# Optimization experiments

Hardware: AMD Instinct MI355X
Metric: run time of the kernel (lower is better)

## Reference

```python
import jax, jax.numpy as jnp
import numpy as np

EPS = 1e-08
STRIDE = 1


def setup_inputs() -> dict:
    key = jax.random.key(0)
    k_x, k_s, k_sw, k_w = jax.random.split(key, 4)
    B, Cin, Cout, D = 8, 32, 32, 48
    style_size, K = 2, 3
    x = jax.random.normal(k_x, (B, Cin, D, D, D), dtype=jnp.float32)
    s = jax.random.normal(k_s, (B, style_size), dtype=jnp.float32)
    # lecun_normal-style scaling for params
    style_weight = jax.random.normal(k_sw, (Cin, style_size), dtype=jnp.float32) / np.sqrt(style_size)
    style_bias = jnp.ones((Cin,), dtype=jnp.float32)
    weight = jax.random.normal(k_w, (Cout, Cin, K, K, K), dtype=jnp.float32) / np.sqrt(Cin * K * K * K)
    bias = jnp.zeros((Cout,), dtype=jnp.float32)
    return {"x": x, "s": s, "style_weight": style_weight,
            "style_bias": style_bias, "weight": weight, "bias": bias}


def reference(x, s, style_weight, style_bias, weight, bias):
    # Style modulation: per-sample per-input-channel scale  (B, Cin)
    s_mod = jnp.dot(s, style_weight.T) + style_bias
    # Modulated weights: (B, Cout, Cin, K, K, K)
    w = weight[None] * s_mod[:, None, :, None, None, None]
    # Demodulation over (Cin, K, K, K) per (B, Cout)
    norm = jnp.sqrt(jnp.sum(w ** 2, axis=(2, 3, 4, 5), keepdims=True) + jnp.float32(EPS))
    w_n = w / norm

    def single_conv(x_i, w_i):
        # x_i: (Cin, D, H, W), w_i: (Cout, Cin, K, K, K)
        out = jax.lax.conv_general_dilated(
            lhs=x_i[None], rhs=w_i,
            window_strides=(STRIDE,) * 3, padding='VALID',
            dimension_numbers=('NCDHW', 'OIDHW', 'NCDHW'))
        return out[0]

    y = jax.vmap(single_conv)(x, w_n)  # (B, Cout, D', H', W')
    return y + bias[None, :, None, None, None]
```

## Files before the change

### kernel.cpp

```cpp
#include <hip/hip_runtime.h>


typedef unsigned short u16;
typedef __bf16 bf16x8 __attribute__((ext_vector_type(8)));
typedef u16 u16x8 __attribute__((ext_vector_type(8)));
typedef float f32x4 __attribute__((ext_vector_type(4)));

#define XT_BYTES  (8u * 110592u * 32u * 2u)
#define WA2_ELEMS (8 * 32 * 27 * 32)

__device__ __forceinline__ u16 f2bf(float f) {
    __bf16 h = (__bf16)f;
    return __builtin_bit_cast(u16, h);
}

__device__ __forceinline__ void dma16(const void* g, void* l) {
    __builtin_amdgcn_global_load_lds(
        (const __attribute__((address_space(1))) unsigned*)g,
        (__attribute__((address_space(3))) unsigned*)l, 16, 0, 0);
}

__global__ __launch_bounds__(256) void xpose_kernel(
    const float* __restrict__ x, u16* __restrict__ xT)
{
    int gid = blockIdx.x * 256 + threadIdx.x;
    int cg   = gid & 3;
    int tmp  = gid >> 2;
    int quad = tmp % 27648;
    int b    = tmp / 27648;
    int site0 = quad * 4;
    const float* xp = x + (size_t)(b * 32 + cg * 8) * 110592 + site0;
    float4 v[8];
#pragma unroll
    for (int j = 0; j < 8; ++j) v[j] = *(const float4*)(xp + (size_t)j * 110592);
#pragma unroll
    for (int k = 0; k < 4; ++k) {
        u16x8 o;
#pragma unroll
        for (int j = 0; j < 8; ++j) o[j] = f2bf(((const float*)&v[j])[k]);
        *(u16x8*)(xT + ((size_t)(b * 110592 + site0 + k) * 4 + cg) * 8) = o;
    }
}

__global__ __launch_bounds__(64) void wnorm32_kernel(
    const float* __restrict__ s, const float* __restrict__ sw,
    const float* __restrict__ sb, const float* __restrict__ w,
    u16* __restrict__ wA2)
{
    int bc = blockIdx.x;
    int b = bc >> 5, co = bc & 31;
    int lane = threadIdx.x;
    float s0 = s[2 * b], s1 = s[2 * b + 1];

    float sum = 0.f;
    for (int i = lane; i < 864; i += 64) {
        int ci = i / 27;
        float m = fmaf(s0, sw[2 * ci], fmaf(s1, sw[2 * ci + 1], sb[ci]));
        float v = w[co * 864 + i] * m;
        sum += v * v;
    }
#pragma unroll
    for (int off = 32; off; off >>= 1) sum += __shfl_xor(sum, off, 64);
    float rn = 1.0f / sqrtf(sum + 1e-8f);

    for (int i = lane; i < 864; i += 64) {
        int ci = i / 27, tap = i - ci * 27;
        float m = fmaf(s0, sw[2 * ci], fmaf(s1, sw[2 * ci + 1], sb[ci]));
        float v = w[co * 864 + i] * m * rn;
        wA2[((size_t)(b * 32 + co) * 27 + tap) * 32 + ci] = f2bf(v);
    }
}

__global__ __launch_bounds__(512) void conv_one(
    const u16* __restrict__ xT, const u16* __restrict__ wA2,
    const float* __restrict__ bias, float* __restrict__ out)
{
    __shared__ u16 sx[57600];

    int orig = blockIdx.x;
    int blk = (orig & 7) * 144 + (orig >> 3);

    int zt = blk % 12, yt = (blk / 12) % 12, b = blk / 144;
    int z0 = zt * 4, y0 = yt * 4;

    int t = threadIdx.x;
    int l = t & 63, w = t >> 6;
    int ln = l & 15;
    int tq = l >> 4;
    int zw = w & 3, yp = (w >> 2) & 1;

#pragma unroll
    for (int i = 0; i < 15; ++i) {
        int idx = i * 512 + t;
        if (idx < 7200) {
            int site = idx >> 2, slot = idx & 3;
            int row = site / 50, x = site - row * 50;
            int zp = row / 6, yq = row - zp * 6;
            int gz = z0 + zp; if (gz > 47) gz = 47;
            int gy = y0 + yq; if (gy > 47) gy = 47;
            int gx = x > 47 ? 47 : x;
            int rot = (row + (x >> 1)) & 3;
            int g = slot ^ rot;
            const u16* src = xT + ((size_t)(b * 110592 + (gz * 48 + gy) * 48 + gx) * 4 + g) * 8;
            dma16(src, (char*)sx + (size_t)idx * 16);
        }
    }
    __syncthreads();

    f32x4 acc[2][3][2];
#pragma unroll
    for (int i = 0; i < 2; i++)
#pragma unroll
        for (int j = 0; j < 3; j++)
#pragma unroll
            for (int h = 0; h < 2; h++) acc[i][j][h] = (f32x4)0.f;

    const u16* wAb = wA2 + (size_t)(b * 32) * 27 * 32;

#pragma unroll
    for (int dz = 0; dz < 3; ++dz) {
#pragma unroll
        for (int dx = 0; dx < 3; ++dx) {
            u16x8 Bf[4][3];
#pragma unroll
            for (int r = 0; r < 4; ++r) {
                int rowi = (zw + dz) * 6 + 2 * yp + r;
#pragma unroll
                for (int xt = 0; xt < 3; ++xt) {
                    int xx = xt * 16 + ln + dx;
                    int site = rowi * 50 + xx;
                    int rot = (rowi + ((ln + dx) >> 1)) & 3;
                    int boff = site * 64 + ((tq ^ rot) << 4);
                    Bf[r][xt] = *(const u16x8*)((const char*)sx + boff);
                }
            }
            u16x8 Af[3][2];
#pragma unroll
            for (int dy = 0; dy < 3; ++dy) {
                int tap = (dz * 3 + dy) * 3 + dx;
#pragma unroll
                for (int h = 0; h < 2; ++h)
                    Af[dy][h] = *(const u16x8*)(wAb
                        + ((size_t)(ln + 16 * h) * 27 + tap) * 32 + tq * 8);
            }
#pragma unroll
            for (int dy = 0; dy < 3; ++dy)
#pragma unroll
                for (int yr = 0; yr < 2; ++yr)
#pragma unroll
                    for (int xt = 0; xt < 3; ++xt)
#pragma unroll
                        for (int h = 0; h < 2; ++h)
                            acc[yr][xt][h] = __builtin_amdgcn_mfma_f32_16x16x32_bf16(
                                __builtin_bit_cast(bf16x8, Af[dy][h]),
                                __builtin_bit_cast(bf16x8, Bf[yr + dy][xt]),
                                acc[yr][xt][h], 0, 0, 0);
        }
    }

    int oz = z0 + zw;
    if (oz < 46) {
#pragma unroll
        for (int yr = 0; yr < 2; ++yr) {
            int oy = y0 + 2 * yp + yr;
            if (oy >= 46) continue;
#pragma unroll
            for (int xt = 0; xt < 3; ++xt) {
                int ox = xt * 16 + ln;
                if (ox >= 46) continue;
#pragma unroll
                for (int h = 0; h < 2; ++h) {
                    f32x4 a = acc[yr][xt][h];
#pragma unroll
                    for (int r = 0; r < 4; ++r) {
                        int co = h * 16 + tq * 4 + r;
                        out[(size_t)(b * 32 + co) * 97336 + oz * 2116 + oy * 46 + ox]
                            = a[r] + bias[co];
                    }
                }
            }
        }
    }
}

__global__ __launch_bounds__(64) void wnorm16_kernel(
    const float* __restrict__ s, const float* __restrict__ sw,
    const float* __restrict__ sb, const float* __restrict__ w,
    u16* __restrict__ wA)
{
    int bc = blockIdx.x;
    int b = bc >> 5, co = bc & 31;
    int lane = threadIdx.x;
    float s0 = s[2 * b], s1 = s[2 * b + 1];

    float sum = 0.f;
    for (int i = lane; i < 864; i += 64) {
        int ci = i / 27;
        float m = fmaf(s0, sw[2 * ci], fmaf(s1, sw[2 * ci + 1], sb[ci]));
        float v = w[co * 864 + i] * m;
        sum += v * v;
    }
#pragma unroll
    for (int off = 32; off; off >>= 1) sum += __shfl_xor(sum, off, 64);
    float rn = 1.0f / sqrtf(sum + 1e-8f);

    for (int i = lane; i < 864; i += 64) {
        int ci = i / 27, tap = i - ci * 27;
        float m = fmaf(s0, sw[2 * ci], fmaf(s1, sw[2 * ci + 1], sb[ci]));
        float v = w[co * 864 + i] * m * rn;
        int chunk = ci >> 4, ci16 = ci & 15;
        wA[(((b * 2 + chunk) * 32 + co) * 28 + tap) * 16 + ci16] = f2bf(v);
    }
    if (lane < 32) {
        int c = lane >> 4, ci16 = lane & 15;
        wA[(((b * 2 + c) * 32 + co) * 28 + 27) * 16 + ci16] = 0;
    }
}

__global__ __launch_bounds__(512) void conv_fallback(
    const float* __restrict__ xin, const u16* __restrict__ wA,
    const float* __restrict__ bias, float* __restrict__ out)
{
    __shared__ u16 sx[28800];

    int blk = blockIdx.x;
    int zt = blk % 12, yt = (blk / 12) % 12, b = blk / 144;
    int z0 = zt * 4, y0 = yt * 4;

    int t = threadIdx.x;
    int l = t & 63, w = t >> 6;
    int ln = l & 15, ch = (l >> 4) & 1, tp = l >> 5, rg = l >> 4;
    int zw = w & 3, yp = w >> 2;

    f32x4 acc[2][3][2];
#pragma unroll
    for (int i = 0; i < 2; i++)
#pragma unroll
        for (int j = 0; j < 3; j++)
#pragma unroll
            for (int h = 0; h < 2; h++) acc[i][j][h] = (f32x4)0.f;

    for (int chunk = 0; chunk < 2; ++chunk) {
        __syncthreads();
        for (int idx = t; idx < 3600; idx += 512) {
            int x = idx % 50;
            int r = idx / 50;
            int cg = r & 1; r >>= 1;
            int y = r % 6, z = r / 6;
            int gz = z0 + z, gy = y0 + y;
            bool inb = (x < 48) && (gy < 48) && (gz < 48);
            const float* xp = xin + (size_t)(b * 32 + chunk * 16 + cg * 8) * 110592
                              + gz * 2304 + gy * 48 + x;
            u16x8 v;
#pragma unroll
            for (int j = 0; j < 8; j++) {
                float f = inb ? xp[(size_t)j * 110592] : 0.f;
                v[j] = f2bf(f);
            }
            *(u16x8*)&sx[idx * 8] = v;
        }
        __syncthreads();

        const u16* wAc = wA + (b * 2 + chunk) * (32 * 28 * 16);
        int aoff = (ln * 28 + tp) * 16 + ch * 8;

#pragma unroll
        for (int s = 0; s < 14; ++s) {
            int tapA = 2 * s + tp;
            bf16x8 A0 = __builtin_bit_cast(bf16x8, *(const u16x8*)(wAc + aoff + s * 32));
            bf16x8 A1 = __builtin_bit_cast(bf16x8, *(const u16x8*)(wAc + aoff + 16 * 28 * 16 + s * 32));
            int tapB = tapA > 26 ? 26 : tapA;
            int dz = tapB / 9;
            int rr = tapB - dz * 9;
            int dy = rr / 3;
            int dx = rr - dy * 3;
            int zr = zw + dz;
#pragma unroll
            for (int yr = 0; yr < 2; ++yr) {
                int yy = 2 * yp + yr + dy;
                int eb = (((zr * 6 + yy) * 2 + ch) * 50 + ln + dx) * 8;
#pragma unroll
                for (int xt = 0; xt < 3; ++xt) {
                    bf16x8 Bf = __builtin_bit_cast(bf16x8, *(const u16x8*)&sx[eb + xt * 128]);
                    acc[yr][xt][0] = __builtin_amdgcn_mfma_f32_16x16x32_bf16(A0, Bf, acc[yr][xt][0], 0, 0, 0);
                    acc[yr][xt][1] = __builtin_amdgcn_mfma_f32_16x16x32_bf16(A1, Bf, acc[yr][xt][1], 0, 0, 0);
                }
            }
        }
    }

    int oz = z0 + zw;
    if (oz < 46) {
#pragma unroll
        for (int yr = 0; yr < 2; ++yr) {
            int oy = y0 + 2 * yp + yr;
            if (oy >= 46) continue;
#pragma unroll
            for (int xt = 0; xt < 3; ++xt) {
                int ox = xt * 16 + ln;
                if (ox >= 46) continue;
#pragma unroll
                for (int h = 0; h < 2; ++h) {
                    f32x4 a = acc[yr][xt][h];
#pragma unroll
                    for (int r = 0; r < 4; ++r) {
                        int co = h * 16 + rg * 4 + r;
                        out[(size_t)(b * 32 + co) * 97336 + oz * 2116 + oy * 46 + ox]
                            = a[r] + bias[co];
                    }
                }
            }
        }
    }
}

extern "C" void kernel_launch(void* const* d_in, const int* in_sizes, int n_in,
                              void* d_out, int out_size, void* d_ws, size_t ws_size,
                              hipStream_t stream) {
    const float* x    = (const float*)d_in[0];
    const float* s    = (const float*)d_in[1];
    const float* sw   = (const float*)d_in[2];
    const float* sb   = (const float*)d_in[3];
    const float* wgt  = (const float*)d_in[4];
    const float* bias = (const float*)d_in[5];
    float* out = (float*)d_out;

    const size_t need = (size_t)XT_BYTES + WA2_ELEMS * sizeof(u16);
    if (ws_size >= need) {
        u16* xT  = (u16*)d_ws;
        u16* wA2 = (u16*)((char*)d_ws + XT_BYTES);
        hipLaunchKernelGGL(xpose_kernel, dim3(3456), dim3(256), 0, stream, x, xT);
        hipLaunchKernelGGL(wnorm32_kernel, dim3(256), dim3(64), 0, stream,
                           s, sw, sb, wgt, wA2);
        hipLaunchKernelGGL(conv_one, dim3(12 * 12 * 8), dim3(512), 0, stream,
                           xT, wA2, bias, out);
    } else {
        u16* wA = (u16*)d_ws;
        hipLaunchKernelGGL(wnorm16_kernel, dim3(256), dim3(64), 0, stream,
                           s, sw, sb, wgt, wA);
        hipLaunchKernelGGL(conv_fallback, dim3(12 * 12 * 8), dim3(512), 0, stream,
                           x, wA, bias, out);
    }
}
```

Baseline: 112.4 us.

## Split conv into two x-range launches with smaller LDS tiles and no swizzle

Replaces the single conv kernel with a templated conv_two launched twice, once for x columns 0-31 (two 16-wide tiles) and once for columns 30-45 (one tile). Each launch stages a narrower LDS slab and declares launch_bounds(512,4), which is meant to raise occupancy and cut register and LDS pressure. The XOR rotation swizzle of the LDS layout is dropped and B/A addresses are precomputed from base pointers to simplify address arithmetic. In exchange it adds a second launch, reloads overlapping halo columns, and may bring back LDS bank conflicts now that the swizzle is gone.

```diff
diff --git a/kernel.cpp b/kernel.cpp
--- a/kernel.cpp
+++ b/kernel.cpp
@@ -71,11 +71,12 @@
     }
 }
 
-__global__ __launch_bounds__(512) void conv_one(
+template<int XTS, int XW, int X0>
+__global__ __launch_bounds__(512, 4) void conv_two(
     const u16* __restrict__ xT, const u16* __restrict__ wA2,
     const float* __restrict__ bias, float* __restrict__ out)
 {
-    __shared__ u16 sx[57600];
+    __shared__ u16 sx[36 * XW * 32];
 
     int orig = blockIdx.x;
     int blk = (orig & 7) * 144 + (orig >> 3);
@@ -87,68 +88,64 @@
     int l = t & 63, w = t >> 6;
     int ln = l & 15;
     int tq = l >> 4;
-    int zw = w & 3, yp = (w >> 2) & 1;
-
-#pragma unroll
-    for (int i = 0; i < 15; ++i) {
+    int zw = w & 3, yp = w >> 2;
+
+    const int NS = 36 * XW * 4;
+#pragma unroll
+    for (int i = 0; i < (NS + 511) / 512; ++i) {
         int idx = i * 512 + t;
-        if (idx < 7200) {
-            int site = idx >> 2, slot = idx & 3;
-            int row = site / 50, x = site - row * 50;
+        if (idx < NS) {
+            int site = idx >> 2, g = idx & 3;
+            int row = site / XW, x = site - row * XW;
             int zp = row / 6, yq = row - zp * 6;
             int gz = z0 + zp; if (gz > 47) gz = 47;
             int gy = y0 + yq; if (gy > 47) gy = 47;
-            int gx = x > 47 ? 47 : x;
-            int rot = (row + (x >> 1)) & 3;
-            int g = slot ^ rot;
+            int gx = X0 + x;  if (gx > 47) gx = 47;
             const u16* src = xT + ((size_t)(b * 110592 + (gz * 48 + gy) * 48 + gx) * 4 + g) * 8;
             dma16(src, (char*)sx + (size_t)idx * 16);
         }
     }
     __syncthreads();
 
-    f32x4 acc[2][3][2];
+    f32x4 acc[2][XTS][2];
 #pragma unroll
     for (int i = 0; i < 2; i++)
 #pragma unroll
-        for (int j = 0; j < 3; j++)
+        for (int j = 0; j < XTS; j++)
 #pragma unroll
             for (int h = 0; h < 2; h++) acc[i][j][h] = (f32x4)0.f;
 
     const u16* wAb = wA2 + (size_t)(b * 32) * 27 * 32;
+    const u16* aB0 = wAb + (size_t)ln * 864 + tq * 8;
+    const u16* aB1 = wAb + (size_t)(ln + 16) * 864 + tq * 8;
+
+    const char* sbase = (const char*)sx
+        + ((size_t)((zw * 6 + 2 * yp) * XW + ln) * 64) + tq * 16;
 
 #pragma unroll
     for (int dz = 0; dz < 3; ++dz) {
 #pragma unroll
         for (int dx = 0; dx < 3; ++dx) {
-            u16x8 Bf[4][3];
-#pragma unroll
-            for (int r = 0; r < 4; ++r) {
-                int rowi = (zw + dz) * 6 + 2 * yp + r;
-#pragma unroll
-                for (int xt = 0; xt < 3; ++xt) {
-                    int xx = xt * 16 + ln + dx;
-                    int site = rowi * 50 + xx;
-                    int rot = (rowi + ((ln + dx) >> 1)) & 3;
-                    int boff = site * 64 + ((tq ^ rot) << 4);
-                    Bf[r][xt] = *(const u16x8*)((const char*)sx + boff);
-                }
-            }
+            u16x8 Bf[4][XTS];
+#pragma unroll
+            for (int r = 0; r < 4; ++r)
+#pragma unroll
+                for (int xt = 0; xt < XTS; ++xt)
+                    Bf[r][xt] = *(const u16x8*)(sbase
+                        + ((dz * 6 + r) * XW + dx + xt * 16) * 64);
             u16x8 Af[3][2];
 #pragma unroll
             for (int dy = 0; dy < 3; ++dy) {
-                int tap = (dz * 3 + dy) * 3 + dx;
-#pragma unroll
-                for (int h = 0; h < 2; ++h)
-                    Af[dy][h] = *(const u16x8*)(wAb
-                        + ((size_t)(ln + 16 * h) * 27 + tap) * 32 + tq * 8);
+                const int tap = (dz * 3 + dy) * 3 + dx;
+                Af[dy][0] = *(const u16x8*)(aB0 + tap * 32);
+                Af[dy][1] = *(const u16x8*)(aB1 + tap * 32);
             }
 #pragma unroll
             for (int dy = 0; dy < 3; ++dy)
 #pragma unroll
                 for (int yr = 0; yr < 2; ++yr)
 #pragma unroll
-                    for (int xt = 0; xt < 3; ++xt)
+                    for (int xt = 0; xt < XTS; ++xt)
 #pragma unroll
                         for (int h = 0; h < 2; ++h)
                             acc[yr][xt][h] = __builtin_amdgcn_mfma_f32_16x16x32_bf16(
@@ -165,8 +162,8 @@
             int oy = y0 + 2 * yp + yr;
             if (oy >= 46) continue;
 #pragma unroll
-            for (int xt = 0; xt < 3; ++xt) {
-                int ox = xt * 16 + ln;
+            for (int xt = 0; xt < XTS; ++xt) {
+                int ox = X0 + xt * 16 + ln;
                 if (ox >= 46) continue;
 #pragma unroll
                 for (int h = 0; h < 2; ++h) {
@@ -281,9 +278,9 @@
                 int eb = (((zr * 6 + yy) * 2 + ch) * 50 + ln + dx) * 8;
 #pragma unroll
                 for (int xt = 0; xt < 3; ++xt) {
-                    bf16x8 Bf = __builtin_bit_cast(bf16x8, *(const u16x8*)&sx[eb + xt * 128]);
-                    acc[yr][xt][0] = __builtin_amdgcn_mfma_f32_16x16x32_bf16(A0, Bf, acc[yr][xt][0], 0, 0, 0);
-                    acc[yr][xt][1] = __builtin_amdgcn_mfma_f32_16x16x32_bf16(A1, Bf, acc[yr][xt][1], 0, 0, 0);
+                    bf16x8 Bf2 = __builtin_bit_cast(bf16x8, *(const u16x8*)&sx[eb + xt * 128]);
+                    acc[yr][xt][0] = __builtin_amdgcn_mfma_f32_16x16x32_bf16(A0, Bf2, acc[yr][xt][0], 0, 0, 0);
+                    acc[yr][xt][1] = __builtin_amdgcn_mfma_f32_16x16x32_bf16(A1, Bf2, acc[yr][xt][1], 0, 0, 0);
                 }
             }
         }
@@ -332,7 +329,9 @@
         hipLaunchKernelGGL(xpose_kernel, dim3(3456), dim3(256), 0, stream, x, xT);
         hipLaunchKernelGGL(wnorm32_kernel, dim3(256), dim3(64), 0, stream,
                            s, sw, sb, wgt, wA2);
-        hipLaunchKernelGGL(conv_one, dim3(12 * 12 * 8), dim3(512), 0, stream,
+        hipLaunchKernelGGL((conv_two<2, 34, 0>), dim3(1152), dim3(512), 0, stream,
+                           xT, wA2, bias, out);
+        hipLaunchKernelGGL((conv_two<1, 18, 30>), dim3(1152), dim3(512), 0, stream,
                            xT, wA2, bias, out);
     } else {
         u16* wA = (u16*)d_ws;
```

After: 138.5 us. +23.2%, slower.
